# Kernel tuning notes

Hardware: AMD Instinct MI355X
Metric: run time of the kernel (lower is better)

## Reference

```python
import jax, jax.numpy as jnp
import numpy as np


def setup_inputs() -> dict:
    key = jax.random.key(0)
    B, C, Nin, Nphi, Nt = 16, 1, 256, 256, 240
    Nout = 2 * Nin
    c0 = 1491.2            # speed of sound in water [m/s]
    L = 0.012              # inner domain half-width [m]
    dx = 2.0 * L / (Nin - 1)
    dt = dx / (2.0 * c0)   # CFL-safe time step
    # sin filter on the outer frequency grid, already in fft (unshifted) order
    k1 = 2.0 * np.pi * np.fft.fftfreq(Nout, d=dx)
    KX, KY = np.meshgrid(k1, k1, indexing='ij')
    knorm = np.sqrt(KX ** 2 + KY ** 2) * (c0 * dt / 2.0)
    sin_filter = (np.sin(knorm) ** 2).astype(np.float32)  # [Nout, Nout]
    # initial pressure
    f = jax.random.normal(key, (B, C, Nin, Nin), dtype=jnp.float32)
    # sensors on a circle in the outer grid (nearest-neighbor indices)
    theta = np.linspace(0.0, 2.0 * np.pi, Nphi, endpoint=False)
    r = Nin // 2 - 2
    idx0 = np.round(Nout // 2 + r * np.cos(theta)).astype(np.int32)
    idx1 = np.round(Nout // 2 + r * np.sin(theta)).astype(np.int32)
    return {
        'f': f,
        'sin_filter': jnp.asarray(sin_filter),
        'idx0': jnp.asarray(idx0),
        'idx1': jnp.asarray(idx1),
        'Nt': Nt,
    }


def reference(f, sin_filter, idx0, idx1, Nt):
    # pad inner grid [B,C,N,N] -> outer grid [B,C,2N,2N] (ConstantPad2d with (Nout-Nin)//2)
    pad = f.shape[-1] // 2
    W0 = jnp.pad(f, ((0, 0), (0, 0), (pad, pad), (pad, pad))).astype(jnp.complex64)
    fil = sin_filter.astype(jnp.complex64)  # broadcast over [B,C,...]

    def step(carry, _):
        W, Walt = carry
        FW = jnp.fft.ifftn(jnp.fft.fftn(W, axes=(-2, -1)) * fil, axes=(-2, -1))
        Wn = 2.0 * W - Walt - 4.0 * FW
        # record updated W at sensor locations (real part): [B,C,Nphi]
        y_i = Wn[:, :, idx0, idx1].real.astype(jnp.float32)
        return (Wn, W), y_i

    (_, _), ys = jax.lax.scan(step, (W0, W0), None, length=Nt)
    # ys: [Nt,B,C,Nphi] -> [B,C,Nphi,Nt]
    return jnp.transpose(ys, (1, 2, 3, 0))
```

## Files before the change

kernel.cpp:

```cpp
#include <hip/hip_runtime.h>
#include <hip/hip_bf16.h>


#define NOUT 512
#define NB 16
#define NPHI 256
#define NT 240
#define RPB 6
#define NGRP 43

#define WREG 5184

typedef float v2f __attribute__((ext_vector_type(2)));
typedef float v4f __attribute__((ext_vector_type(4)));
typedef unsigned int v2u __attribute__((ext_vector_type(2)));

__device__ __forceinline__ v2f cmulv(v2f a, v2f b) {
    return v2f{fmaf(a.x, b.x, -a.y * b.y), fmaf(a.x, b.y, a.y * b.x)};
}
__device__ __forceinline__ v2f cmuliv(v2f a) { return v2f{-a.y, a.x}; }
__device__ __forceinline__ v2f cmulw8v(v2f a) {
    const float s = 0.70710678118654752f; return v2f{s * (a.x - a.y), s * (a.x + a.y)};
}
__device__ __forceinline__ v2f cmulw83v(v2f a) {
    const float s = 0.70710678118654752f; return v2f{-s * (a.x + a.y), s * (a.x - a.y)};
}

__device__ __forceinline__ void dft8p(const v2f y[8], v2f Y[8]) {
    v2f t0 = y[0] + y[4], t4 = y[0] - y[4];
    v2f t1 = y[1] + y[5], t5 = cmulw8v(y[1] - y[5]);
    v2f t2 = y[2] + y[6], t6 = cmuliv(y[2] - y[6]);
    v2f t3 = y[3] + y[7], t7 = cmulw83v(y[3] - y[7]);
    v2f u0 = t0 + t2, u2 = t0 - t2;
    v2f u1 = t1 + t3, u3 = cmuliv(t1 - t3);
    Y[0] = u0 + u1; Y[4] = u0 - u1;
    Y[2] = u2 + u3; Y[6] = u2 - u3;
    v2f v0 = t4 + t6, v2 = t4 - t6;
    v2f v1 = t5 + t7, v3 = cmuliv(t5 - t7);
    Y[1] = v0 + v1; Y[5] = v0 - v1;
    Y[3] = v2 + v3; Y[7] = v2 - v3;
}

__device__ __forceinline__ void dft8p_ip(v2f y[8]) {
    v2f t0 = y[0] + y[4], t4 = y[0] - y[4];
    v2f t1 = y[1] + y[5], t5 = cmulw8v(y[1] - y[5]);
    v2f t2 = y[2] + y[6], t6 = cmuliv(y[2] - y[6]);
    v2f t3 = y[3] + y[7], t7 = cmulw83v(y[3] - y[7]);
    v2f u0 = t0 + t2, u2 = t0 - t2;
    v2f u1 = t1 + t3, u3 = cmuliv(t1 - t3);
    y[0] = u0 + u1; y[4] = u0 - u1;
    y[2] = u2 + u3; y[6] = u2 - u3;
    v2f v0 = t4 + t6, v2 = t4 - t6;
    v2f v1 = t5 + t7, v3 = cmuliv(t5 - t7);
    y[1] = v0 + v1; y[5] = v0 - v1;
    y[3] = v2 + v3; y[7] = v2 - v3;
}

__device__ __forceinline__ v2f wlookup(const float2* trig, int m) {
    m &= 511;
    float2 ph = trig[m & 255];
    return (m & 256) ? v2f{-ph.x, -ph.y} : v2f{ph.x, ph.y};
}

template<int CTRL>
__device__ __forceinline__ float dppx(float x) {
    return __int_as_float(__builtin_amdgcn_mov_dpp(__float_as_int(x), CTRL, 0xF, 0xF, true));
}
__device__ __forceinline__ float swzx4(float x) {
    return __int_as_float(__builtin_amdgcn_ds_swizzle(__float_as_int(x), 0x101F));
}

template<int CTRL>
__device__ __forceinline__ void xchg_dpp(v2f& a, v2f& b, bool bit) {
    float sx = bit ? a.x : b.x;
    float sy = bit ? a.y : b.y;
    float tx = dppx<CTRL>(sx);
    float ty = dppx<CTRL>(sy);
    a.x = bit ? tx : a.x;   a.y = bit ? ty : a.y;
    b.x = bit ? b.x : tx;   b.y = bit ? b.y : ty;
}
__device__ __forceinline__ void xchg_swz4(v2f& a, v2f& b, bool bit) {
    float sx = bit ? a.x : b.x;
    float sy = bit ? a.y : b.y;
    float tx = swzx4(sx);
    float ty = swzx4(sy);
    a.x = bit ? tx : a.x;   a.y = bit ? ty : a.y;
    b.x = bit ? b.x : tx;   b.y = bit ? b.y : ty;
}

#if __has_builtin(__builtin_amdgcn_permlane16_swap)
__device__ __forceinline__ void pl16x(v2f& a, v2f& b) {
    v2u rx = __builtin_amdgcn_permlane16_swap(__float_as_uint(a.x), __float_as_uint(b.x), false, false);
    a.x = __uint_as_float(rx.x); b.x = __uint_as_float(rx.y);
    v2u ry = __builtin_amdgcn_permlane16_swap(__float_as_uint(a.y), __float_as_uint(b.y), false, false);
    a.y = __uint_as_float(ry.x); b.y = __uint_as_float(ry.y);
}
#else
__device__ __forceinline__ void pl16x(v2f& a, v2f& b) {
    bool bit = (threadIdx.x & 16) != 0;
    float sx = bit ? a.x : b.x, sy = bit ? a.y : b.y;
    float tx = __shfl_xor(sx, 16), ty = __shfl_xor(sy, 16);
    a.x = bit ? tx : a.x; a.y = bit ? ty : a.y;
    b.x = bit ? b.x : tx; b.y = bit ? b.y : ty;
}
#endif

#if __has_builtin(__builtin_amdgcn_permlane32_swap)
__device__ __forceinline__ void pl32x(v2f& a, v2f& b) {
    v2u rx = __builtin_amdgcn_permlane32_swap(__float_as_uint(a.x), __float_as_uint(b.x), false, false);
    a.x = __uint_as_float(rx.x); b.x = __uint_as_float(rx.y);
    v2u ry = __builtin_amdgcn_permlane32_swap(__float_as_uint(a.y), __float_as_uint(b.y), false, false);
    a.y = __uint_as_float(ry.x); b.y = __uint_as_float(ry.y);
}
#else
__device__ __forceinline__ void pl32x(v2f& a, v2f& b) {
    bool bit = (threadIdx.x & 32) != 0;
    float sx = bit ? a.x : b.x, sy = bit ? a.y : b.y;
    float tx = __shfl_xor(sx, 32), ty = __shfl_xor(sy, 32);
    a.x = bit ? tx : a.x; a.y = bit ? ty : a.y;
    b.x = bit ? b.x : tx; b.y = bit ? b.y : ty;
}
#endif

__device__ __forceinline__ void fft_sample(
    const v2f y[8], const v2f tA[8], const v2f tB[8],
    bool b0, bool b1, bool b2, bool b3,
    char* awBase, const char* ldsBase, int spos, const v2f ph[RPB], bool active,
    float* pA)
{
    v2f G[8];
    dft8p(y, G);
#pragma unroll
    for (int k1 = 1; k1 < 8; ++k1) G[k1] = cmulv(G[k1], tA[k1]);
    xchg_dpp<0x128>(G[0], G[1], b3);  xchg_dpp<0x128>(G[2], G[3], b3);
    xchg_dpp<0x128>(G[4], G[5], b3);  xchg_dpp<0x128>(G[6], G[7], b3);
    pl16x(G[0], G[2]);  pl16x(G[1], G[3]);  pl16x(G[4], G[6]);  pl16x(G[5], G[7]);
    pl32x(G[0], G[4]);  pl32x(G[1], G[5]);  pl32x(G[2], G[6]);  pl32x(G[3], G[7]);
    dft8p_ip(G);
#pragma unroll
    for (int m1 = 1; m1 < 8; ++m1) G[m1] = cmulv(G[m1], tB[m1]);
    xchg_dpp<0xB1>(G[0], G[1], b0);  xchg_dpp<0xB1>(G[2], G[3], b0);
    xchg_dpp<0xB1>(G[4], G[5], b0);  xchg_dpp<0xB1>(G[6], G[7], b0);
    xchg_dpp<0x4E>(G[0], G[2], b1);  xchg_dpp<0x4E>(G[1], G[3], b1);
    xchg_dpp<0x4E>(G[4], G[6], b1);  xchg_dpp<0x4E>(G[5], G[7], b1);
    xchg_swz4(G[0], G[4], b2);  xchg_swz4(G[1], G[5], b2);
    xchg_swz4(G[2], G[6], b2);  xchg_swz4(G[3], G[7], b2);
    dft8p_ip(G);
    __syncthreads();
    *(v4f*)(awBase +  0) = v4f{G[0].x, G[0].y, G[1].x, G[1].y};
    *(v4f*)(awBase + 16) = v4f{G[2].x, G[2].y, G[3].x, G[3].y};
    *(v4f*)(awBase + 32) = v4f{G[4].x, G[4].y, G[5].x, G[5].y};
    *(v4f*)(awBase + 48) = v4f{G[6].x, G[6].y, G[7].x, G[7].y};
    __syncthreads();
    if (active) {
        float acc = 0.0f;
#pragma unroll
        for (int ww = 0; ww < RPB; ++ww) {
            v2f q = *(const v2f*)(ldsBase + ww * WREG + spos);
            acc = fmaf(q.x, ph[ww].x, fmaf(-q.y, ph[ww].y, acc));
        }
        pA[0] = acc;
    }
}

__device__ __forceinline__ void cbfly(float& ar, float& ai, float& br, float& bi,
                                      float wr, float wi) {
    float dr = ar - br, di = ai - bi;
    ar = ar + br; ai = ai + bi;
    br = fmaf(dr, wr, -di * wi);
    bi = fmaf(dr, wi,  di * wr);
}

__device__ __forceinline__ void init_trig(float2* trig, int tid) {
    if (tid < 256) {
        float ang = (float)tid * (6.283185307179586f / 512.0f);
        float s, c;
        sincosf(ang, &s, &c);
        trig[tid] = make_float2(c, s);
    }
}

__device__ __forceinline__ void fft512_inv_lds(float* xr, float* xi, const float2* trig, int L) {
#pragma unroll
    for (int r = 0; r < 4; ++r) {
        float2 w = trig[(r << 6) + L];
        cbfly(xr[r], xi[r], xr[r + 4], xi[r + 4], w.x, w.y);
    }
    {
        float2 w0 = trig[L << 1];
        float2 w1 = trig[(64 + L) << 1];
        cbfly(xr[0], xi[0], xr[2], xi[2], w0.x, w0.y);
        cbfly(xr[1], xi[1], xr[3], xi[3], w1.x, w1.y);
        cbfly(xr[4], xi[4], xr[6], xi[6], w0.x, w0.y);
        cbfly(xr[5], xi[5], xr[7], xi[7], w1.x, w1.y);
    }
    {
        float2 w = trig[L << 2];
        cbfly(xr[0], xi[0], xr[1], xi[1], w.x, w.y);
        cbfly(xr[2], xi[2], xr[3], xi[3], w.x, w.y);
        cbfly(xr[4], xi[4], xr[5], xi[5], w.x, w.y);
        cbfly(xr[6], xi[6], xr[7], xi[7], w.x, w.y);
    }
#pragma unroll
    for (int s = 3; s <= 8; ++s) {
        const int half = 512 >> (s + 1);
        const int ex = (L & (half - 1)) << s;
        float2 w = trig[ex];
        const bool hi = (L & half) != 0;
        float wr = hi ? w.x : 1.0f;
        float wi = hi ? w.y : 0.0f;
        float sg = hi ? -1.0f : 1.0f;
#pragma unroll
        for (int r = 0; r < 8; ++r) {
            float orv = __shfl_xor(xr[r], half);
            float oiv = __shfl_xor(xi[r], half);
            float tr = fmaf(sg, xr[r], orv);
            float ti = fmaf(sg, xi[r], oiv);
            xr[r] = fmaf(tr, wr, -ti * wi);
            xi[r] = fmaf(tr, wi,  ti * wr);
        }
    }
}

__global__ __launch_bounds__(256) void f1_kernel(const float* __restrict__ f,
                                                 float2* __restrict__ R) {
    __shared__ float2 trig[256];
    const int tid = threadIdx.x;
    init_trig(trig, tid);
    __syncthreads();
    const int w = tid >> 6, L = tid & 63;
    const int x = 128 + blockIdx.x * 4 + w;
    const int b = blockIdx.y;
    const float* frow = f + ((size_t)b * 256 + (x - 128)) * 256;
    float xr[8], xi[8];
#pragma unroll
    for (int r = 0; r < 8; ++r) {
        int e = r * 64 + L;
        xr[r] = (e >= 128 && e < 384) ? frow[e - 128] : 0.0f;
        xi[r] = 0.0f;
    }
    fft512_inv_lds(xr, xi, trig, L);
    float2* Rrow = R + ((size_t)b * NOUT + x) * NOUT;
#pragma unroll
    for (int r = 0; r < 8; ++r) {
        int e = r * 64 + L;
        int k = __brev((unsigned)e) >> 23;
        Rrow[k] = make_float2(xr[r], -xi[r]);
    }
}

__global__ __launch_bounds__(256) void f2_kernel(const float2* __restrict__ R,
                                                 float2* __restrict__ A0) {
    __shared__ float2 trig[256];
    const int tid = threadIdx.x;
    init_trig(trig, tid);
    __syncthreads();
    const int w = tid >> 6, L = tid & 63;
    const int q = blockIdx.x * 4 + w;
    const int b = blockIdx.y;
    float xr[8], xi[8];
#pragma unroll
    for (int r = 0; r < 8; ++r) {
        if (r >= 2 && r < 6) {
            int e = r * 64 + L;
            float2 v = R[((size_t)b * NOUT + e) * NOUT + q];
            xr[r] = v.x;
            xi[r] = -v.y;
        } else {
            xr[r] = 0.0f;
            xi[r] = 0.0f;
        }
    }
    fft512_inv_lds(xr, xi, trig, L);
#pragma unroll
    for (int r = 0; r < 8; ++r) {
        int e = r * 64 + L;
        int p = __brev((unsigned)e) >> 23;
        A0[((size_t)b * NOUT + p) * NOUT + q] = make_float2(xr[r], -xi[r]);
    }
}

__global__ __launch_bounds__(384, 4) void sim_kernel(
    const float* __restrict__ fil,
    const int* __restrict__ idx0, const int* __restrict__ idx1,
    float2* __restrict__ stateCur, float2* __restrict__ statePrev,
    float* __restrict__ partial, int Tc, int firstChunk, int lastChunk)
{
    __shared__ __align__(16) char waveMem[RPB * WREG];
    __shared__ float2 trig[256];

    const int tid = threadIdx.x;
    const int w = tid >> 6, L = tid & 63;
    const int g = blockIdx.x, b = blockIdx.y;
    const int p = g * RPB + w;

    if (tid < 256) {
        float ang = (float)tid * (6.283185307179586f / 512.0f);
        float s, c;
        sincosf(ang, &s, &c);
        trig[tid] = make_float2(c, s);
    }
    __syncthreads();

    v2f tA[8], tB[8];
#pragma unroll
    for (int k1 = 1; k1 < 8; ++k1) tA[k1] = wlookup(trig, L * k1);
#pragma unroll
    for (int m1 = 1; m1 < 8; ++m1) tB[m1] = wlookup(trig, 8 * (L & 7) * m1);

    const bool b0 = (L & 1) != 0;
    const bool b1 = (L & 2) != 0;
    const bool b2 = (L & 4) != 0;
    const bool b3 = (L & 8) != 0;

    const bool active = tid < 256;
    int spos = 0;
    v2f ph[RPB];
    if (active) {
        int u = idx0[tid];
        int v = idx1[tid];
        spos = ((v & 7) * 8 + ((v >> 3) & 7)) * 80 + (v >> 6) * 8;
#pragma unroll
        for (int ww = 0; ww < RPB; ++ww) {
            int prow = g * RPB + ww;
            v2f a0;
            if (prow == 0)        a0 = v2f{1.0f, 0.0f};
            else if (prow == 256) a0 = v2f{(u & 1) ? -1.0f : 1.0f, 0.0f};
            else if (prow == 257) a0 = v2f{0.0f, 0.0f};
            else                  a0 = 2.0f * wlookup(trig, prow * u);
            ph[ww] = a0;
        }
    } else {
#pragma unroll
        for (int ww = 0; ww < RPB; ++ww) ph[ww] = v2f{0.0f, 0.0f};
    }

    char* myA    = waveMem + w * WREG;
    char* awBase = myA + L * 80;

    v2f a[8], bb[8];
    float C[8];
    {
        const size_t rowBase = ((size_t)b * NOUT + p) * NOUT;
        const float* filRow = fil + (size_t)p * NOUT;
#pragma unroll
        for (int r = 0; r < 8; ++r) {
            int e = r * 64 + L;
            float2 a0 = stateCur[rowBase + e];
            a[r] = v2f{a0.x, a0.y};
            if (firstChunk) {
                bb[r] = a[r];
            } else {
                float2 a1 = statePrev[rowBase + e];
                bb[r] = v2f{a1.x, a1.y};
            }
            C[r] = fmaf(-4.0f, filRow[e], 2.0f);
        }
    }

    float* pOut = partial + ((size_t)g * Tc * NB + b) * NPHI + tid;

    for (int tl = 0; tl < Tc; tl += 2) {
#pragma unroll
        for (int r = 0; r < 8; ++r) bb[r] = v2f{C[r], C[r]} * a[r] - bb[r];
        fft_sample(bb, tA, tB, b0, b1, b2, b3, awBase,
                   waveMem, spos, ph, active, pOut);
        pOut += NB * NPHI;
#pragma unroll
        for (int r = 0; r < 8; ++r) a[r] = v2f{C[r], C[r]} * bb[r] - a[r];
        fft_sample(a, tA, tB, b0, b1, b2, b3, awBase,
                   waveMem, spos, ph, active, pOut);
        pOut += NB * NPHI;
    }

    if (!lastChunk) {
        const size_t rowBase = ((size_t)b * NOUT + p) * NOUT;
#pragma unroll
        for (int r = 0; r < 8; ++r) {
            int e = r * 64 + L;
            stateCur[rowBase + e]  = make_float2(a[r].x, a[r].y);
            statePrev[rowBase + e] = make_float2(bb[r].x, bb[r].y);
        }
    }
}

__global__ __launch_bounds__(256) void reduce_kernel(const float* __restrict__ partial,
                                                     float* __restrict__ out,
                                                     int Tc, int tStart) {
    int id = blockIdx.x * 256 + threadIdx.x;
    int j = id & 255;
    int b = (id >> 8) & 15;
    int tl = id >> 12;
    float s = 0.0f;
#pragma unroll
    for (int gg = 0; gg < NGRP; ++gg)
        s += partial[(((size_t)gg * Tc + tl) * NB + b) * NPHI + j];
    out[((size_t)b * NPHI + j) * NT + (tStart + tl)] = s * (1.0f / (512.0f * 512.0f));
}

extern "C" void kernel_launch(void* const* d_in, const int* in_sizes, int n_in,
                              void* d_out, int out_size, void* d_ws, size_t ws_size,
                              hipStream_t stream) {
    (void)in_sizes; (void)n_in; (void)out_size;
    const float* f   = (const float*)d_in[0];
    const float* fil = (const float*)d_in[1];
    const int* idx0  = (const int*)d_in[2];
    const int* idx1  = (const int*)d_in[3];
    float* out = (float*)d_out;

    char* ws = (char*)d_ws;
    const size_t stateBytes = (size_t)NB * NOUT * NOUT * sizeof(float2);
    float2* stateCur  = (float2*)ws;
    float2* statePrev = (float2*)(ws + stateBytes);
    float*  partial   = (float*)(ws + 2 * stateBytes);
    size_t remain = (ws_size > 2 * stateBytes) ? ws_size - 2 * stateBytes : 0;

    static const int tcs[] = {240, 120, 80, 60, 48, 40, 30, 24, 20, 16, 12, 10, 8, 6, 4, 2};
    int Tc = 2;
    for (int i = 0; i < 16; ++i) {
        size_t need = (size_t)NGRP * tcs[i] * NB * NPHI * sizeof(float);
        if (need <= remain) { Tc = tcs[i]; break; }
    }

    f1_kernel<<<dim3(64, NB), 256, 0, stream>>>(f, statePrev);
    f2_kernel<<<dim3(128, NB), 256, 0, stream>>>(statePrev, stateCur);
    for (int t0 = 0; t0 < NT; t0 += Tc) {
        int last = (t0 + Tc) >= NT ? 1 : 0;
        sim_kernel<<<dim3(NGRP, NB), RPB * 64, 0, stream>>>(fil, idx0, idx1, stateCur, statePrev,
                                                            partial, Tc, t0 == 0 ? 1 : 0, last);
        reduce_kernel<<<dim3(Tc * NB), 256, 0, stream>>>(partial, out, Tc, t0);
    }
}
```

Baseline: 974.4 us.

## Compute only sensor-needed FFT outputs and double-buffer LDS to drop a barrier

The final radix-8 stage now computes only the four outputs whose column indices can hold sensor positions, and writes half as much data to LDS. The sensor read offset is shifted to match the narrower layout. Consecutive time steps alternate between two LDS offsets, which removes the barrier before the write. This cuts ALU work, LDS traffic and one barrier per step. It relies on the sensor columns falling only in that range and on the offset buffers not overlapping.

After: 950.2 us. -2.5%, faster.

```diff
diff --git a/kernel.cpp b/kernel.cpp
--- a/kernel.cpp
+++ b/kernel.cpp
@@ -56,6 +56,21 @@
     y[3] = v2 + v3; y[7] = v2 - v3;
 }
 
+__device__ __forceinline__ void dft8p_mid4(const v2f y[8], v2f o[4]) {
+    v2f t0 = y[0] + y[4], t4 = y[0] - y[4];
+    v2f t1 = y[1] + y[5], t5 = cmulw8v(y[1] - y[5]);
+    v2f t2 = y[2] + y[6], t6 = cmuliv(y[2] - y[6]);
+    v2f t3 = y[3] + y[7], t7 = cmulw83v(y[3] - y[7]);
+    v2f u0 = t0 + t2, u2 = t0 - t2;
+    v2f u1 = t1 + t3, u3 = cmuliv(t1 - t3);
+    v2f w0 = t4 + t6, w2 = t4 - t6;
+    v2f w1 = t5 + t7, w3 = cmuliv(t5 - t7);
+    o[0] = u2 + u3;
+    o[1] = w2 + w3;
+    o[2] = u0 - u1;
+    o[3] = w0 - w1;
+}
+
 __device__ __forceinline__ v2f wlookup(const float2* trig, int m) {
     m &= 511;
     float2 ph = trig[m & 255];
@@ -145,12 +160,10 @@
     xchg_dpp<0x4E>(G[4], G[6], b1);  xchg_dpp<0x4E>(G[5], G[7], b1);
     xchg_swz4(G[0], G[4], b2);  xchg_swz4(G[1], G[5], b2);
     xchg_swz4(G[2], G[6], b2);  xchg_swz4(G[3], G[7], b2);
-    dft8p_ip(G);
-    __syncthreads();
-    *(v4f*)(awBase +  0) = v4f{G[0].x, G[0].y, G[1].x, G[1].y};
-    *(v4f*)(awBase + 16) = v4f{G[2].x, G[2].y, G[3].x, G[3].y};
-    *(v4f*)(awBase + 32) = v4f{G[4].x, G[4].y, G[5].x, G[5].y};
-    *(v4f*)(awBase + 48) = v4f{G[6].x, G[6].y, G[7].x, G[7].y};
+    v2f o[4];
+    dft8p_mid4(G, o);
+    *(v4f*)(awBase +  0) = v4f{o[0].x, o[0].y, o[1].x, o[1].y};
+    *(v4f*)(awBase + 16) = v4f{o[2].x, o[2].y, o[3].x, o[3].y};
     __syncthreads();
     if (active) {
         float acc = 0.0f;
@@ -319,7 +332,7 @@
     if (active) {
         int u = idx0[tid];
         int v = idx1[tid];
-        spos = ((v & 7) * 8 + ((v >> 3) & 7)) * 80 + (v >> 6) * 8;
+        spos = ((v & 7) * 8 + ((v >> 3) & 7)) * 80 + ((v >> 6) * 8 - 16);
 #pragma unroll
         for (int ww = 0; ww < RPB; ++ww) {
             int prow = g * RPB + ww;
@@ -363,13 +376,13 @@
     for (int tl = 0; tl < Tc; tl += 2) {
 #pragma unroll
         for (int r = 0; r < 8; ++r) bb[r] = v2f{C[r], C[r]} * a[r] - bb[r];
-        fft_sample(bb, tA, tB, b0, b1, b2, b3, awBase,
-                   waveMem, spos, ph, active, pOut);
+        fft_sample(bb, tA, tB, b0, b1, b2, b3, awBase, waveMem,
+                   spos, ph, active, pOut);
         pOut += NB * NPHI;
 #pragma unroll
         for (int r = 0; r < 8; ++r) a[r] = v2f{C[r], C[r]} * bb[r] - a[r];
-        fft_sample(a, tA, tB, b0, b1, b2, b3, awBase,
-                   waveMem, spos, ph, active, pOut);
+        fft_sample(a, tA, tB, b0, b1, b2, b3, awBase + 32, waveMem + 32,
+                   spos, ph, active, pOut);
         pOut += NB * NPHI;
     }
 
```
